# Performance work log

Measured on AMD Instinct MI355X. Metric: run time of the kernel, lower is better.

Reference implementation:

```python
import jax, jax.numpy as jnp
import numpy as np

B, T, D, H = 16, 2048, 1024, 1024  # batch, seq (effective block_size), n_embed, head_size


def setup_inputs() -> dict:
    key = jax.random.key(0)
    k1, k2, k3, k4 = jax.random.split(key, 4)
    x = jax.random.normal(k1, (B, T, D), dtype=jnp.float32)
    # torch Linear weight is [out,in]; store as [in,out] for x @ W
    s = 1.0 / np.sqrt(D)
    Wq = jax.random.uniform(k2, (D, H), dtype=jnp.float32, minval=-s, maxval=s)
    Wk = jax.random.uniform(k3, (D, H), dtype=jnp.float32, minval=-s, maxval=s)
    Wv = jax.random.uniform(k4, (D, H), dtype=jnp.float32, minval=-s, maxval=s)
    return {"x": x, "Wq": Wq, "Wk": Wk, "Wv": Wv}


def reference(x, Wq, Wk, Wv):
    # Single-head causal self-attention, NO 1/sqrt(d) scaling (faithful to source).
    q = x @ Wq  # [B,T,H]
    k = x @ Wk  # [B,T,H]
    v = x @ Wv  # [B,T,H]
    w = jnp.einsum('bth,bsh->bts', q, k)  # [B,T,T]
    Tn = x.shape[1]
    causal = jnp.tril(jnp.ones((Tn, Tn), dtype=bool))
    w = jnp.where(causal, w, -jnp.inf)
    w = jax.nn.softmax(w, axis=-1)
    # dropout is identity in eval mode
    out = jnp.einsum('bts,bsh->bth', w, v)  # [B,T,H]
    return out
```

## Files before the change

### kernel.cpp

```cpp
#include <hip/hip_runtime.h>
#include <hip/hip_bf16.h>


typedef _Float16 half8 __attribute__((ext_vector_type(8)));
typedef _Float16 half4v __attribute__((ext_vector_type(4)));
typedef float floatx4 __attribute__((ext_vector_type(4)));

#define TB 16
#define TT 2048
#define TD 1024

#define BARRIER() asm volatile("s_barrier" ::: "memory")

__global__ void cvt_f32_f16(const float* __restrict__ in, _Float16* __restrict__ out, long n) {
    long i = ((long)blockIdx.x * blockDim.x + threadIdx.x) * 4;
    long stride = (long)gridDim.x * blockDim.x * 4;
    for (; i < n; i += stride) {
        float4 f = *(const float4*)(in + i);
        half4v h;
        h[0] = (_Float16)f.x; h[1] = (_Float16)f.y;
        h[2] = (_Float16)f.z; h[3] = (_Float16)f.w;
        *(half4v*)(out + i) = h;
    }
}

__global__ void transpose_cvt_w(const float* __restrict__ in, _Float16* __restrict__ out) {
    __shared__ float tile[32][33];
    const int bx = blockIdx.x * 32, by = blockIdx.y * 32;
    const int tx = threadIdx.x, ty = threadIdx.y;
#pragma unroll
    for (int i = ty; i < 32; i += 8) tile[i][tx] = in[(long)(by + i) * 1024 + bx + tx];
    __syncthreads();
#pragma unroll
    for (int i = ty; i < 32; i += 8) out[(long)(bx + i) * 1024 + by + tx] = (_Float16)tile[tx][i];
}

__device__ __forceinline__ void gload16(const _Float16* g, _Float16* l) {
    __builtin_amdgcn_global_load_lds((const __attribute__((address_space(1))) void*)g,
                                     (__attribute__((address_space(3))) void*)l, 16, 0, 0);
}

template <int MODE>
__global__ __launch_bounds__(512, 2) void gemm256(const _Float16* __restrict__ A,
                                                  const _Float16* __restrict__ B,
                                                  void* __restrict__ Cout,
                                                  void* __restrict__ Cout2,
                                                  int K, int lda, int ldb, int ldc,
                                                  long sAb, long sBb, long sCb,
                                                  int tilesN, int tilesM, int nb) {
    __shared__ _Float16 lds[49152];
    const int tid = threadIdx.x, lane = tid & 63, w = tid >> 6;
    const int wr = w >> 2, wc = w & 3;

    int b, ti, tj;
    if (MODE == 2) {
        const int grp = nb * 4;
        const int g = blockIdx.x / grp;
        ti = tilesM - 1 - g;
        int i2 = blockIdx.x - g * grp;
        const int q = grp >> 3, r = grp & 7, xcd = i2 & 7, idx = i2 >> 3;
        i2 = (xcd < r ? xcd * (q + 1) : r * (q + 1) + (xcd - r) * q) + idx;
        b = i2 >> 2; tj = i2 & 3;
    } else {
        int bx = blockIdx.x;
        const int nwg = gridDim.x, q = nwg >> 3, r = nwg & 7, xcd = bx & 7, idx = bx >> 3;
        bx = (xcd < r ? xcd * (q + 1) : r * (q + 1) + (xcd - r) * q) + idx;
        b = blockIdx.y;
        if (MODE == 1) {
            int rd = bx; ti = 0;
            while (rd > ti) { rd -= ti + 1; ++ti; }
            tj = rd;
        } else {
            ti = bx / tilesN; tj = bx % tilesN;
        }
    }
    A += (long)b * sAb;
    B += (long)b * sBb;
    const long m0 = (long)ti * 256, n0 = (long)tj * 256;
    const int nkt = (MODE == 2) ? (ti + 1) * 8 : (K >> 5);

    const int row0 = tid >> 2;
    const int co   = (((tid & 3) ^ ((tid >> 3) & 3)) << 3);
    const int fcol = ((((lane >> 4) ^ (lane >> 1)) & 3) << 3);
    const int arow = wr * 128 + (lane & 15);
    const int brow = wc * 64 + (lane & 15);

    auto Abase = [&](int buf) { return lds + (buf << 13); };
    auto Bbase = [&](int buf) { return lds + 24576 + (buf << 13); };

    auto stageA = [&](int buf, int kt) {
        const long kb = (long)kt * 32 + co;
        _Float16* d = Abase(buf) + (w << 9);
        gload16(A + (m0 + row0) * (long)lda + kb, d);
        gload16(A + (m0 + row0 + 128) * (long)lda + kb, d + 4096);
    };
    auto stageB = [&](int buf, int kt) {
        const long kb = (long)kt * 32 + co;
        _Float16* d = Bbase(buf) + (w << 9);
        gload16(B + (n0 + row0) * (long)ldb + kb, d);
        gload16(B + (n0 + row0 + 128) * (long)ldb + kb, d + 4096);
    };
    auto ldA = [&](int buf, int m) {
        return *(const half8*)(Abase(buf) + (arow + m * 16) * 32 + fcol);
    };
    auto ldB = [&](int buf, int n) {
        return *(const half8*)(Bbase(buf) + (brow + n * 16) * 32 + fcol);
    };

    floatx4 acc[8][4] = {};
    half8 af[8], bf[4];

    {
        const int k1 = (1 < nkt) ? 1 : 0;
        stageA(0, 0); stageB(0, 0);
        stageA(1, k1); stageB(1, k1);
    }
    asm volatile("s_waitcnt vmcnt(4)" ::: "memory");
    BARRIER();

    int cur = 0;
    for (int t = 0; t < nkt; ++t) {
        const int b2 = (cur + 2 >= 3) ? cur - 1 : cur + 2;
        const int kt2 = (t + 2 < nkt) ? t + 2 : nkt - 1;
#pragma unroll
        for (int nn = 0; nn < 4; ++nn) bf[nn] = ldB(cur, nn);
#pragma unroll
        for (int mm = 0; mm < 8; ++mm) af[mm] = ldA(cur, mm);
        stageA(b2, kt2); stageB(b2, kt2);
        __builtin_amdgcn_s_setprio(1);
#pragma unroll
        for (int mm = 0; mm < 4; ++mm)
#pragma unroll
            for (int nn = 0; nn < 4; ++nn)
                acc[mm][nn] = __builtin_amdgcn_mfma_f32_16x16x32_f16(af[mm], bf[nn], acc[mm][nn], 0, 0, 0);
#pragma unroll
        for (int mm = 4; mm < 8; ++mm)
#pragma unroll
            for (int nn = 0; nn < 4; ++nn)
                acc[mm][nn] = __builtin_amdgcn_mfma_f32_16x16x32_f16(af[mm], bf[nn], acc[mm][nn], 0, 0, 0);
        __builtin_amdgcn_s_setprio(0);
        asm volatile("s_waitcnt vmcnt(4)" ::: "memory");
        BARRIER();
        cur = (cur + 1 >= 3) ? 0 : cur + 1;
    }
    asm volatile("s_waitcnt vmcnt(0) lgkmcnt(0)" ::: "memory");

    const int r4 = (lane >> 4) * 4, ccol = lane & 15;
    if (MODE != 2) {
        _Float16* C;
        long nb0 = n0;
        if (MODE == 3 && n0 >= TD) { C = (_Float16*)Cout2; nb0 = n0 - TD; }
        else                        C = (_Float16*)Cout + (long)b * sCb;
#pragma unroll
        for (int m = 0; m < 8; ++m) {
            const long rbase = m0 + wr * 128 + m * 16 + r4;
#pragma unroll
            for (int n = 0; n < 4; ++n) {
                const long cbase = nb0 + wc * 64 + n * 16 + ccol;
#pragma unroll
                for (int j = 0; j < 4; ++j)
                    C[(rbase + j) * (long)ldc + cbase] = (_Float16)acc[m][n][j];
            }
        }
    } else {
        float* C = (float*)Cout + (long)b * sCb;
#pragma unroll
        for (int m = 0; m < 8; ++m) {
            const long rbase = m0 + wr * 128 + m * 16 + r4;
#pragma unroll
            for (int n = 0; n < 4; ++n) {
                const long cbase = n0 + wc * 64 + n * 16 + ccol;
#pragma unroll
                for (int j = 0; j < 4; ++j)
                    C[(rbase + j) * (long)ldc + cbase] = acc[m][n][j];
            }
        }
    }
}

__global__ __launch_bounds__(256) void softmax_rows_f16(_Float16* __restrict__ S, int T) {
    const int wv = threadIdx.x >> 6, lane = threadIdx.x & 63;
    const long row = (long)blockIdx.x * 4 + wv;
    const int t = (int)(row & (T - 1));
    _Float16* s = S + row * (long)T;
    const int nstore = ((t >> 8) + 1) << 8;

    float v[4][8];
    float mx = -__builtin_inff();
#pragma unroll
    for (int c = 0; c < 4; ++c) {
        const int col0 = (c * 64 + lane) * 8;
        if (col0 <= t) {
            half8 hv = *(const half8*)(s + col0);
#pragma unroll
            for (int j = 0; j < 8; ++j) {
                v[c][j] = (col0 + j <= t) ? (float)hv[j] : -__builtin_inff();
                mx = fmaxf(mx, v[c][j]);
            }
        } else {
#pragma unroll
            for (int j = 0; j < 8; ++j) v[c][j] = -__builtin_inff();
        }
    }
#pragma unroll
    for (int o = 32; o; o >>= 1) mx = fmaxf(mx, __shfl_xor(mx, o));

    float sum = 0.f;
#pragma unroll
    for (int c = 0; c < 4; ++c)
#pragma unroll
        for (int j = 0; j < 8; ++j) {
            float p = __expf(v[c][j] - mx);
            v[c][j] = p;
            sum += p;
        }
#pragma unroll
    for (int o = 32; o; o >>= 1) sum += __shfl_xor(sum, o);
    const float inv = 1.f / sum;

#pragma unroll
    for (int c = 0; c < 4; ++c) {
        const int col0 = (c * 64 + lane) * 8;
        if (col0 < nstore) {
            half8 o;
#pragma unroll
            for (int j = 0; j < 8; ++j) o[j] = (_Float16)(v[c][j] * inv);
            *(half8*)(s + col0) = o;
        }
    }
}

extern "C" void kernel_launch(void* const* d_in, const int* in_sizes, int n_in,
                              void* d_out, int out_size, void* d_ws, size_t ws_size,
                              hipStream_t stream) {
    const float* x  = (const float*)d_in[0];
    const float* Wq = (const float*)d_in[1];
    const float* Wk = (const float*)d_in[2];
    const float* Wv = (const float*)d_in[3];
    float* out = (float*)d_out;

    const size_t XB = (size_t)TB * TT * TD;

    _Float16* x16 = (_Float16*)d_out;
    _Float16* Kh  = (_Float16*)d_out + XB;

    char* ws = (char*)d_ws;
    size_t off = 0;
    auto carve = [&](size_t bytes) { char* p = ws + off; off = (off + bytes + 255) & ~(size_t)255; return p; };
    _Float16* wqt = (_Float16*)carve((size_t)TD * TD * 2);
    _Float16* wkt = (_Float16*)carve((size_t)TD * TD * 2);
    _Float16* wvt = (_Float16*)carve((size_t)TD * TD * 2);
    _Float16* Qh  = (_Float16*)carve(XB * 2);
    _Float16* Vt  = (_Float16*)carve(XB * 2);

    const size_t CH = (size_t)TT * TT * 2;
    int NB = 16;
    while (NB > 1 && off + (size_t)NB * CH > ws_size) NB >>= 1;
    _Float16* Sc = (_Float16*)carve((size_t)NB * CH);

    cvt_f32_f16<<<2048, 256, 0, stream>>>(x, x16, (long)XB);
    transpose_cvt_w<<<dim3(32, 32), dim3(32, 8), 0, stream>>>(Wq, wqt);
    transpose_cvt_w<<<dim3(32, 32), dim3(32, 8), 0, stream>>>(Wk, wkt);
    transpose_cvt_w<<<dim3(32, 32), dim3(32, 8), 0, stream>>>(Wv, wvt);

    gemm256<3><<<dim3(128 * 8, 1), 512, 0, stream>>>(x16, wqt, Qh, Kh, TD, TD, TD, TD,
                                                     0, 0, 0, 8, 128, 0);
    gemm256<0><<<dim3(4 * 8, TB), 512, 0, stream>>>(wvt, x16, Vt, nullptr, TD, TD, TD, TT,
                                                    0, (long)TT * TD, (long)TD * TT, 8, 4, 0);

    for (int cb = 0; cb < TB; cb += NB) {
        gemm256<1><<<dim3(36, NB), 512, 0, stream>>>(Qh + (size_t)cb * TT * TD,
                                                     Kh + (size_t)cb * TT * TD, Sc, nullptr,
                                                     TD, TD, TD, TT,
                                                     (long)TT * TD, (long)TT * TD, (long)TT * TT, 8, 8, 0);
        softmax_rows_f16<<<NB * TT / 4, 256, 0, stream>>>(Sc, TT);
        gemm256<2><<<dim3(NB * 32, 1), 512, 0, stream>>>(Sc, Vt + (size_t)cb * TD * TT,
                                                         out + (size_t)cb * TT * TD, nullptr, TT,
                                                         TT, TT, TD,
                                                         (long)TT * TT, (long)TD * TT, (long)TT * TD, 4, 8, NB);
    }
}
```

Measured before the change: 485.2 us.

## Use 1024-thread GEMM blocks with 64x64 warp tiles and split-K double buffering

The 256x256 GEMM kernel now runs with 16 waves per block instead of 8, so each wave computes a 64x64 sub-tile with half the accumulators. The K loop now covers 64 elements per iteration, split into two 32-wide halves. Two LDS buffers of two halves each replace the old three-stage ring, which raises LDS use to 128 KB. The goal is more latency hiding from extra waves and finer interleaving of loads with MFMA work. The cost is one resident block per CU, more barriers per unit of work, and a tight register budget under launch_bounds(1024,4), which could cause spills.

```diff
diff --git a/kernel.cpp b/kernel.cpp
--- a/kernel.cpp
+++ b/kernel.cpp
@@ -41,14 +41,14 @@
 }
 
 template <int MODE>
-__global__ __launch_bounds__(512, 2) void gemm256(const _Float16* __restrict__ A,
-                                                  const _Float16* __restrict__ B,
-                                                  void* __restrict__ Cout,
-                                                  void* __restrict__ Cout2,
-                                                  int K, int lda, int ldb, int ldc,
-                                                  long sAb, long sBb, long sCb,
-                                                  int tilesN, int tilesM, int nb) {
-    __shared__ _Float16 lds[49152];
+__global__ __launch_bounds__(1024, 4) void gemm256(const _Float16* __restrict__ A,
+                                                   const _Float16* __restrict__ B,
+                                                   void* __restrict__ Cout,
+                                                   void* __restrict__ Cout2,
+                                                   int K, int lda, int ldb, int ldc,
+                                                   long sAb, long sBb, long sCb,
+                                                   int tilesN, int tilesM, int nb) {
+    __shared__ _Float16 lds[65536];
     const int tid = threadIdx.x, lane = tid & 63, w = tid >> 6;
     const int wr = w >> 2, wc = w & 3;
 
@@ -77,71 +77,73 @@
     A += (long)b * sAb;
     B += (long)b * sBb;
     const long m0 = (long)ti * 256, n0 = (long)tj * 256;
-    const int nkt = (MODE == 2) ? (ti + 1) * 8 : (K >> 5);
+    const int nkt = (MODE == 2) ? (ti + 1) * 4 : (K >> 6);
 
     const int row0 = tid >> 2;
     const int co   = (((tid & 3) ^ ((tid >> 3) & 3)) << 3);
     const int fcol = ((((lane >> 4) ^ (lane >> 1)) & 3) << 3);
-    const int arow = wr * 128 + (lane & 15);
+    const int arow = wr * 64 + (lane & 15);
     const int brow = wc * 64 + (lane & 15);
 
-    auto Abase = [&](int buf) { return lds + (buf << 13); };
-    auto Bbase = [&](int buf) { return lds + 24576 + (buf << 13); };
-
-    auto stageA = [&](int buf, int kt) {
-        const long kb = (long)kt * 32 + co;
-        _Float16* d = Abase(buf) + (w << 9);
-        gload16(A + (m0 + row0) * (long)lda + kb, d);
-        gload16(A + (m0 + row0 + 128) * (long)lda + kb, d + 4096);
-    };
-    auto stageB = [&](int buf, int kt) {
-        const long kb = (long)kt * 32 + co;
-        _Float16* d = Bbase(buf) + (w << 9);
-        gload16(B + (n0 + row0) * (long)ldb + kb, d);
-        gload16(B + (n0 + row0 + 128) * (long)ldb + kb, d + 4096);
-    };
-    auto ldA = [&](int buf, int m) {
-        return *(const half8*)(Abase(buf) + (arow + m * 16) * 32 + fcol);
-    };
-    auto ldB = [&](int buf, int n) {
-        return *(const half8*)(Bbase(buf) + (brow + n * 16) * 32 + fcol);
-    };
-
-    floatx4 acc[8][4] = {};
-    half8 af[8], bf[4];
-
-    {
-        const int k1 = (1 < nkt) ? 1 : 0;
-        stageA(0, 0); stageB(0, 0);
-        stageA(1, k1); stageB(1, k1);
-    }
+    auto Abase = [&](int buf, int kk) { return lds + ((buf * 2 + kk) << 13); };
+    auto Bbase = [&](int buf, int kk) { return lds + 32768 + ((buf * 2 + kk) << 13); };
+
+    auto stageA = [&](int buf, int kk, int kt) {
+        gload16(A + (m0 + row0) * (long)lda + (long)kt * 64 + kk * 32 + co,
+                Abase(buf, kk) + (w << 9));
+    };
+    auto stageB = [&](int buf, int kk, int kt) {
+        gload16(B + (n0 + row0) * (long)ldb + (long)kt * 64 + kk * 32 + co,
+                Bbase(buf, kk) + (w << 9));
+    };
+    auto ldA = [&](int buf, int kk, int m) {
+        return *(const half8*)(Abase(buf, kk) + (arow + m * 16) * 32 + fcol);
+    };
+    auto ldB = [&](int buf, int kk, int n) {
+        return *(const half8*)(Bbase(buf, kk) + (brow + n * 16) * 32 + fcol);
+    };
+
+    floatx4 acc[4][4] = {};
+    half8 af[4], bf[4];
+
+    stageA(0, 0, 0); stageB(0, 0, 0);
+    stageA(0, 1, 0); stageB(0, 1, 0);
+    stageA(1, 0, 1); stageB(1, 0, 1);
     asm volatile("s_waitcnt vmcnt(4)" ::: "memory");
     BARRIER();
 
-    int cur = 0;
     for (int t = 0; t < nkt; ++t) {
-        const int b2 = (cur + 2 >= 3) ? cur - 1 : cur + 2;
+        const int cur = t & 1, nxt = cur ^ 1;
+        const int kt1 = (t + 1 < nkt) ? t + 1 : nkt - 1;
         const int kt2 = (t + 2 < nkt) ? t + 2 : nkt - 1;
-#pragma unroll
-        for (int nn = 0; nn < 4; ++nn) bf[nn] = ldB(cur, nn);
-#pragma unroll
-        for (int mm = 0; mm < 8; ++mm) af[mm] = ldA(cur, mm);
-        stageA(b2, kt2); stageB(b2, kt2);
+        stageA(nxt, 1, kt1); stageB(nxt, 1, kt1);
+#pragma unroll
+        for (int nn = 0; nn < 4; ++nn) bf[nn] = ldB(cur, 0, nn);
+#pragma unroll
+        for (int mm = 0; mm < 4; ++mm) af[mm] = ldA(cur, 0, mm);
         __builtin_amdgcn_s_setprio(1);
 #pragma unroll
         for (int mm = 0; mm < 4; ++mm)
-#pragma unroll
-            for (int nn = 0; nn < 4; ++nn)
-                acc[mm][nn] = __builtin_amdgcn_mfma_f32_16x16x32_f16(af[mm], bf[nn], acc[mm][nn], 0, 0, 0);
-#pragma unroll
-        for (int mm = 4; mm < 8; ++mm)
 #pragma unroll
             for (int nn = 0; nn < 4; ++nn)
                 acc[mm][nn] = __builtin_amdgcn_mfma_f32_16x16x32_f16(af[mm], bf[nn], acc[mm][nn], 0, 0, 0);
         __builtin_amdgcn_s_setprio(0);
         asm volatile("s_waitcnt vmcnt(4)" ::: "memory");
         BARRIER();
-        cur = (cur + 1 >= 3) ? 0 : cur + 1;
+        stageA(cur, 0, kt2); stageB(cur, 0, kt2);
+#pragma unroll
+        for (int nn = 0; nn < 4; ++nn) bf[nn] = ldB(cur, 1, nn);
+#pragma unroll
+        for (int mm = 0; mm < 4; ++mm) af[mm] = ldA(cur, 1, mm);
+        __builtin_amdgcn_s_setprio(1);
+#pragma unroll
+        for (int mm = 0; mm < 4; ++mm)
+#pragma unroll
+            for (int nn = 0; nn < 4; ++nn)
+                acc[mm][nn] = __builtin_amdgcn_mfma_f32_16x16x32_f16(af[mm], bf[nn], acc[mm][nn], 0, 0, 0);
+        __builtin_amdgcn_s_setprio(0);
+        asm volatile("s_waitcnt vmcnt(4)" ::: "memory");
+        BARRIER();
     }
     asm volatile("s_waitcnt vmcnt(0) lgkmcnt(0)" ::: "memory");
 
@@ -152,8 +154,8 @@
         if (MODE == 3 && n0 >= TD) { C = (_Float16*)Cout2; nb0 = n0 - TD; }
         else                        C = (_Float16*)Cout + (long)b * sCb;
 #pragma unroll
-        for (int m = 0; m < 8; ++m) {
-            const long rbase = m0 + wr * 128 + m * 16 + r4;
+        for (int m = 0; m < 4; ++m) {
+            const long rbase = m0 + wr * 64 + m * 16 + r4;
 #pragma unroll
             for (int n = 0; n < 4; ++n) {
                 const long cbase = nb0 + wc * 64 + n * 16 + ccol;
@@ -165,8 +167,8 @@
     } else {
         float* C = (float*)Cout + (long)b * sCb;
 #pragma unroll
-        for (int m = 0; m < 8; ++m) {
-            const long rbase = m0 + wr * 128 + m * 16 + r4;
+        for (int m = 0; m < 4; ++m) {
+            const long rbase = m0 + wr * 64 + m * 16 + r4;
 #pragma unroll
             for (int n = 0; n < 4; ++n) {
                 const long cbase = n0 + wc * 64 + n * 16 + ccol;
@@ -263,20 +265,20 @@
     transpose_cvt_w<<<dim3(32, 32), dim3(32, 8), 0, stream>>>(Wk, wkt);
     transpose_cvt_w<<<dim3(32, 32), dim3(32, 8), 0, stream>>>(Wv, wvt);
 
-    gemm256<3><<<dim3(128 * 8, 1), 512, 0, stream>>>(x16, wqt, Qh, Kh, TD, TD, TD, TD,
-                                                     0, 0, 0, 8, 128, 0);
-    gemm256<0><<<dim3(4 * 8, TB), 512, 0, stream>>>(wvt, x16, Vt, nullptr, TD, TD, TD, TT,
-                                                    0, (long)TT * TD, (long)TD * TT, 8, 4, 0);
+    gemm256<3><<<dim3(128 * 8, 1), 1024, 0, stream>>>(x16, wqt, Qh, Kh, TD, TD, TD, TD,
+                                                      0, 0, 0, 8, 128, 0);
+    gemm256<0><<<dim3(4 * 8, TB), 1024, 0, stream>>>(wvt, x16, Vt, nullptr, TD, TD, TD, TT,
+                                                     0, (long)TT * TD, (long)TD * TT, 8, 4, 0);
 
     for (int cb = 0; cb < TB; cb += NB) {
-        gemm256<1><<<dim3(36, NB), 512, 0, stream>>>(Qh + (size_t)cb * TT * TD,
-                                                     Kh + (size_t)cb * TT * TD, Sc, nullptr,
-                                                     TD, TD, TD, TT,
-                                                     (long)TT * TD, (long)TT * TD, (long)TT * TT, 8, 8, 0);
+        gemm256<1><<<dim3(36, NB), 1024, 0, stream>>>(Qh + (size_t)cb * TT * TD,
+                                                      Kh + (size_t)cb * TT * TD, Sc, nullptr,
+                                                      TD, TD, TD, TT,
+                                                      (long)TT * TD, (long)TT * TD, (long)TT * TT, 8, 8, 0);
         softmax_rows_f16<<<NB * TT / 4, 256, 0, stream>>>(Sc, TT);
-        gemm256<2><<<dim3(NB * 32, 1), 512, 0, stream>>>(Sc, Vt + (size_t)cb * TD * TT,
-                                                         out + (size_t)cb * TT * TD, nullptr, TT,
-                                                         TT, TT, TD,
-                                                         (long)TT * TT, (long)TD * TT, (long)TT * TD, 4, 8, NB);
-    }
-}
+        gemm256<2><<<dim3(NB * 32, 1), 1024, 0, stream>>>(Sc, Vt + (size_t)cb * TD * TT,
+                                                          out + (size_t)cb * TT * TD, nullptr, TT,
+                                                          TT, TT, TD,
+                                                          (long)TT * TT, (long)TD * TT, (long)TT * TD, 4, 8, NB);
+    }
+}
```

New measurement: 487.0 us. Within noise of the previous version (+0.4%).

## Deepen GEMM LDS pipeline to four stages and split each K step into halves

Applied to the files above, without the earlier changes.

Grows the shared-memory ring from three to four K-slices and prefetches three slices ahead instead of two. Each iteration is split into two MFMA halves, with the A-slice prefetch issued before the first half and the B-slice prefetch before the second. A barrier between the halves spreads global-to-LDS traffic across the loop, and only four A fragments are held in registers at a time. The cost is 128 KB of LDS per block instead of 96 KB, plus one extra barrier per K step.

```diff
diff --git a/kernel.cpp b/kernel.cpp
--- a/kernel.cpp
+++ b/kernel.cpp
@@ -48,7 +48,7 @@
                                                   int K, int lda, int ldb, int ldc,
                                                   long sAb, long sBb, long sCb,
                                                   int tilesN, int tilesM, int nb) {
-    __shared__ _Float16 lds[49152];
+    __shared__ _Float16 lds[65536];
     const int tid = threadIdx.x, lane = tid & 63, w = tid >> 6;
     const int wr = w >> 2, wc = w & 3;
 
@@ -77,7 +77,7 @@
     A += (long)b * sAb;
     B += (long)b * sBb;
     const long m0 = (long)ti * 256, n0 = (long)tj * 256;
-    const int nkt = (MODE == 2) ? (ti + 1) * 8 : (K >> 5);
+    const int nh = (MODE == 2) ? (ti + 1) * 8 : (K >> 5);
 
     const int row0 = tid >> 2;
     const int co   = (((tid & 3) ^ ((tid >> 3) & 3)) << 3);
@@ -85,64 +85,68 @@
     const int arow = wr * 128 + (lane & 15);
     const int brow = wc * 64 + (lane & 15);
 
-    auto Abase = [&](int buf) { return lds + (buf << 13); };
-    auto Bbase = [&](int buf) { return lds + 24576 + (buf << 13); };
-
-    auto stageA = [&](int buf, int kt) {
-        const long kb = (long)kt * 32 + co;
-        _Float16* d = Abase(buf) + (w << 9);
+    auto Abase = [&](int slot) { return lds + (slot << 13); };
+    auto Bbase = [&](int slot) { return lds + 32768 + (slot << 13); };
+
+    auto stageA = [&](int slot, int kh) {
+        const long kb = (long)kh * 32 + co;
+        _Float16* d = Abase(slot) + (w << 9);
         gload16(A + (m0 + row0) * (long)lda + kb, d);
         gload16(A + (m0 + row0 + 128) * (long)lda + kb, d + 4096);
     };
-    auto stageB = [&](int buf, int kt) {
-        const long kb = (long)kt * 32 + co;
-        _Float16* d = Bbase(buf) + (w << 9);
+    auto stageB = [&](int slot, int kh) {
+        const long kb = (long)kh * 32 + co;
+        _Float16* d = Bbase(slot) + (w << 9);
         gload16(B + (n0 + row0) * (long)ldb + kb, d);
         gload16(B + (n0 + row0 + 128) * (long)ldb + kb, d + 4096);
     };
-    auto ldA = [&](int buf, int m) {
-        return *(const half8*)(Abase(buf) + (arow + m * 16) * 32 + fcol);
-    };
-    auto ldB = [&](int buf, int n) {
-        return *(const half8*)(Bbase(buf) + (brow + n * 16) * 32 + fcol);
+    auto ldA = [&](int slot, int m) {
+        return *(const half8*)(Abase(slot) + (arow + m * 16) * 32 + fcol);
+    };
+    auto ldB = [&](int slot, int n) {
+        return *(const half8*)(Bbase(slot) + (brow + n * 16) * 32 + fcol);
     };
 
     floatx4 acc[8][4] = {};
-    half8 af[8], bf[4];
+    half8 af[4], bf[4];
+
+#define MFMA16(MH)                                                                     \
+    _Pragma("unroll") for (int mm = 0; mm < 4; ++mm)                                   \
+    _Pragma("unroll") for (int nn = 0; nn < 4; ++nn)                                   \
+        acc[(MH)*4 + mm][nn] =                                                         \
+            __builtin_amdgcn_mfma_f32_16x16x32_f16(af[mm], bf[nn], acc[(MH)*4 + mm][nn], 0, 0, 0);
 
     {
-        const int k1 = (1 < nkt) ? 1 : 0;
+        const int k1 = (1 < nh) ? 1 : nh - 1, k2 = (2 < nh) ? 2 : nh - 1;
         stageA(0, 0); stageB(0, 0);
         stageA(1, k1); stageB(1, k1);
-    }
-    asm volatile("s_waitcnt vmcnt(4)" ::: "memory");
+        stageA(2, k2); stageB(2, k2);
+    }
+    asm volatile("s_waitcnt vmcnt(8)" ::: "memory");
     BARRIER();
 
-    int cur = 0;
-    for (int t = 0; t < nkt; ++t) {
-        const int b2 = (cur + 2 >= 3) ? cur - 1 : cur + 2;
-        const int kt2 = (t + 2 < nkt) ? t + 2 : nkt - 1;
-#pragma unroll
-        for (int nn = 0; nn < 4; ++nn) bf[nn] = ldB(cur, nn);
-#pragma unroll
-        for (int mm = 0; mm < 8; ++mm) af[mm] = ldA(cur, mm);
-        stageA(b2, kt2); stageB(b2, kt2);
+    for (int h = 0; h < nh; ++h) {
+        const int s = h & 3, s3 = (h + 3) & 3;
+        const int kh3 = (h + 3 < nh) ? h + 3 : nh - 1;
+        stageA(s3, kh3);
+#pragma unroll
+        for (int nn = 0; nn < 4; ++nn) bf[nn] = ldB(s, nn);
+#pragma unroll
+        for (int mm = 0; mm < 4; ++mm) af[mm] = ldA(s, mm);
         __builtin_amdgcn_s_setprio(1);
-#pragma unroll
-        for (int mm = 0; mm < 4; ++mm)
-#pragma unroll
-            for (int nn = 0; nn < 4; ++nn)
-                acc[mm][nn] = __builtin_amdgcn_mfma_f32_16x16x32_f16(af[mm], bf[nn], acc[mm][nn], 0, 0, 0);
-#pragma unroll
-        for (int mm = 4; mm < 8; ++mm)
-#pragma unroll
-            for (int nn = 0; nn < 4; ++nn)
-                acc[mm][nn] = __builtin_amdgcn_mfma_f32_16x16x32_f16(af[mm], bf[nn], acc[mm][nn], 0, 0, 0);
+        MFMA16(0)
         __builtin_amdgcn_s_setprio(0);
-        asm volatile("s_waitcnt vmcnt(4)" ::: "memory");
         BARRIER();
-        cur = (cur + 1 >= 3) ? 0 : cur + 1;
-    }
+        stageB(s3, kh3);
+#pragma unroll
+        for (int mm = 0; mm < 4; ++mm) af[mm] = ldA(s, mm + 4);
+        __builtin_amdgcn_s_setprio(1);
+        MFMA16(1)
+        __builtin_amdgcn_s_setprio(0);
+        asm volatile("s_waitcnt vmcnt(8)" ::: "memory");
+        BARRIER();
+    }
+#undef MFMA16
     asm volatile("s_waitcnt vmcnt(0) lgkmcnt(0)" ::: "memory");
 
     const int r4 = (lane >> 4) * 4, ccol = lane & 15;
```

New measurement: 486.5 us. About the same (+0.3%).
